# Performance work log

Measured on AMD Instinct MI355X. Metric: run time of the kernel, lower is better.

## Reference

```python
import jax, jax.numpy as jnp
import numpy as np

HIDDEN = 4096
FFN = 14336
GS = 64  # groupsize


def dequant2(qw, scales, zeros, N):
    """Unpack 2-bit HQQ weights. qw: (N//4, K) int32, scales/zeros: (G, K).
    Returns W of shape (N, K) float: (bits - zeros[n % G]) * scales[n % G]."""
    G = scales.shape[0]
    n = jnp.arange(N)
    packed = qw[n // 4]                      # (N, K)
    shift = ((3 - (n % 4)) * 2).astype(qw.dtype)  # per-row bit shift
    vals = (packed >> shift[:, None]) & 3    # (N, K) 2-bit codes
    g = n % G
    return (vals.astype(scales.dtype) - zeros[g]) * scales[g]


def setup_inputs() -> dict:
    key = jax.random.key(0)
    ks = jax.random.split(key, 12)
    x = jax.random.normal(ks[0], (512, HIDDEN), dtype=jnp.float32)
    qw1 = jax.random.randint(ks[1], (FFN // 4, HIDDEN), 0, 256, dtype=jnp.int32)
    qw3 = jax.random.randint(ks[2], (FFN // 4, HIDDEN), 0, 256, dtype=jnp.int32)
    qw2 = jax.random.randint(ks[3], (HIDDEN // 4, FFN), 0, 256, dtype=jnp.int32)
    G1 = FFN // GS
    G2 = HIDDEN // GS
    s1 = jax.random.uniform(ks[4], (G1, HIDDEN), dtype=jnp.float32) * 0.05
    z1 = jax.random.uniform(ks[5], (G1, HIDDEN), dtype=jnp.float32)
    s3 = jax.random.uniform(ks[6], (G1, HIDDEN), dtype=jnp.float32) * 0.05
    z3 = jax.random.uniform(ks[7], (G1, HIDDEN), dtype=jnp.float32)
    s2 = jax.random.uniform(ks[8], (G2, FFN), dtype=jnp.float32) * 0.05
    z2 = jax.random.uniform(ks[9], (G2, FFN), dtype=jnp.float32)
    return {"x": x, "qw1": qw1, "s1": s1, "z1": z1, "qw3": qw3, "s3": s3,
            "z3": z3, "qw2": qw2, "s2": s2, "z2": z2, "groupsize": GS}


def reference(x, qw1, s1, z1, qw3, s3, z3, qw2, s2, z2, groupsize):
    # gate / up projections: C = x @ W^T, W dequantized to (N, K)
    w1 = dequant2(qw1, s1, z1, FFN)      # (FFN, HIDDEN)
    w3 = dequant2(qw3, s3, z3, FFN)      # (FFN, HIDDEN)
    w2 = dequant2(qw2, s2, z2, HIDDEN)   # (HIDDEN, FFN)
    gate = jnp.einsum('mk,nk->mn', x, w1)   # (M, FFN)
    up = jnp.einsum('mk,nk->mn', x, w3)     # (M, FFN)
    h = jax.nn.silu(gate) * up               # SwiGLU
    out = jnp.einsum('mf,hf->mh', h, w2)     # (M, HIDDEN)
    return out
```

## Files before the change

### kernel.cpp

```cpp
#include <hip/hip_runtime.h>
#include <hip/hip_fp16.h>
#include <stdint.h>

#define HIDDEN 4096
#define FFN    14336
#define MDIM   512
#define G1     224
#define G2     64
#define BK     64
#define KB_H   128
#define KB_F   448

typedef _Float16 f16x8 __attribute__((ext_vector_type(8)));
typedef float f32x4 __attribute__((ext_vector_type(4)));

#define SCHED0() __builtin_amdgcn_sched_barrier(0);
#define LGKM_BAR()                                            \
    asm volatile("s_waitcnt lgkmcnt(0)" ::: "memory");        \
    __builtin_amdgcn_s_barrier();                             \
    __builtin_amdgcn_sched_barrier(0);


__global__ void cvt_xp_kernel(const float* __restrict__ x, ushort* __restrict__ xbp) {
    int i = blockIdx.x * blockDim.x + threadIdx.x;
    int ls = i & 63;
    int kb = (i >> 6) & (KB_H - 1);
    int mb = i >> 13;
    int row = mb * 16 + (ls & 15);
    int col = kb * 32 + (ls >> 4) * 8;
    const float4* src = (const float4*)&x[(size_t)row * HIDDEN + col];
    float4 v0 = src[0], v1 = src[1];
    __half2 h0 = __floats2half2_rn(v0.x, v0.y);
    __half2 h1 = __floats2half2_rn(v0.z, v0.w);
    __half2 h2 = __floats2half2_rn(v1.x, v1.y);
    __half2 h3 = __floats2half2_rn(v1.z, v1.w);
    uint4 o = make_uint4(__builtin_bit_cast(uint32_t, h0), __builtin_bit_cast(uint32_t, h1),
                         __builtin_bit_cast(uint32_t, h2), __builtin_bit_cast(uint32_t, h3));
    ((uint4*)xbp)[i] = o;
}

__global__ void build_sz_kernel(const float* __restrict__ s, const float* __restrict__ z,
                                uint32_t* __restrict__ outp) {
    int i = blockIdx.x * blockDim.x + threadIdx.x;
    float s0 = s[2 * i], s1 = s[2 * i + 1];
    float z0 = z[2 * i], z1 = z[2 * i + 1];
    __half2 hs = __floats2half2_rn(s0, s1);
    __half2 hn = __floats2half2_rn(-z0 * s0, -z1 * s1);
    ((uint2*)outp)[i] = make_uint2(__builtin_bit_cast(uint32_t, hs),
                                   __builtin_bit_cast(uint32_t, hn));
}

__device__ __forceinline__ uint32_t deq2(uint32_t w0, uint32_t w1, uint32_t sh,
                                         uint32_t spair, uint32_t npair) {
    uint32_t c0 = (w0 >> sh) & 3u;
    uint32_t c1 = (w1 >> sh) & 3u;
    uint32_t sel = 0x01000100u + c0 * 0x0202u + c1 * 0x02020000u;
    uint32_t codes = __builtin_amdgcn_perm(0x42004000u, 0x3C000000u, sel);
    __half2 r = __hfma2(__builtin_bit_cast(__half2, codes),
                        __builtin_bit_cast(__half2, spair),
                        __builtin_bit_cast(__half2, npair));
    return __builtin_bit_cast(uint32_t, r);
}


__global__ __launch_bounds__(256, 2)
void gemm_gateup(const ushort* __restrict__ xbp, const uint32_t* __restrict__ qw1,
                 const uint32_t* __restrict__ sz1, const uint32_t* __restrict__ qw3,
                 const uint32_t* __restrict__ sz3, ushort* __restrict__ hp) {
    __shared__ ushort sB1[2][32 * 64];
    __shared__ ushort sB2[2][32 * 64];
    __shared__ ushort sE[256 * 32];

    const int tid = threadIdx.x;
    const int idx = ((blockIdx.x & 7) * 112) + (blockIdx.x >> 3);
    const int mt = idx & 1, nt = idx >> 1;
    const int m0 = mt * 256, n0 = nt * 32;

    const int lane = tid & 63, w = tid >> 6;
    const int wm = w * 64;
    const int frow = lane & 15, fk = (lane >> 4) * 8;
    const int sw = (frow & 7) << 3;

    uint32_t abase[4];
#pragma unroll
    for (int mi = 0; mi < 4; ++mi)
        abase[mi] = (uint32_t)(((m0 >> 4) + w * 4 + mi) * KB_H) * 512 + lane * 8;

    const int bi = tid & 127;
    const int rp = bi >> 3;
    const int kc = (bi & 7) * 8;
    const int row0 = rp * 2;
    const int g0 = (n0 + row0) % G1;
    const uint32_t* qp = (tid < 128 ? qw1 : qw3) + (size_t)(n0 / 4 + (rp >> 1)) * HIDDEN + kc;
    const uint32_t* zp = (tid < 128 ? sz1 : sz3) + (size_t)g0 * HIDDEN + kc;
    ushort (*sB)[32 * 64] = (tid < 128) ? sB1 : sB2;
    const uint32_t sh0 = 6u - 4u * (uint32_t)(rp & 1);

    f32x4 accG[4][2], accU[4][2];
#pragma unroll
    for (int i = 0; i < 4; ++i)
#pragma unroll
        for (int j = 0; j < 2; ++j) {
            accG[i][j] = (f32x4){0.f, 0.f, 0.f, 0.f};
            accU[i][j] = (f32x4){0.f, 0.f, 0.f, 0.f};
        }

    f16x8 afA[8], afB[8];
    uint4 pwA0, pwA1, pzA0, pzA1, pzA2, pzA3;
    uint4 pwB0, pwB1, pzB0, pzB1, pzB2, pzB3;

#define GU_LDA(AF, tt)                                                         \
    { _Pragma("unroll")                                                        \
      for (int mi = 0; mi < 4; ++mi)                                           \
          _Pragma("unroll")                                                    \
          for (int kk = 0; kk < 2; ++kk)                                       \
              AF[mi * 2 + kk] =                                                \
                  *(const f16x8*)&xbp[abase[mi] + (uint32_t)((tt) * 2 + kk) * 512]; }

#define GU_LD(PW0, PW1, PZ0, PZ1, PZ2, PZ3, k0q)                               \
    PW0 = *(const uint4*)(qp + (k0q));                                         \
    PW1 = *(const uint4*)(qp + (k0q) + 4);                                     \
    PZ0 = *(const uint4*)(zp + (k0q));                                         \
    PZ1 = *(const uint4*)(zp + (k0q) + 4);                                     \
    PZ2 = *(const uint4*)(zp + HIDDEN + (k0q));                                \
    PZ3 = *(const uint4*)(zp + HIDDEN + (k0q) + 4);

#define GU_DEQ(wbuf, PW0, PW1, PZ0, PZ1, PZ2, PZ3)                             \
    { const uint32_t wv[8] = {(PW0).x, (PW0).y, (PW0).z, (PW0).w,              \
                              (PW1).x, (PW1).y, (PW1).z, (PW1).w};             \
      {   const uint32_t sp[4] = {(PZ0).x, (PZ0).z, (PZ1).x, (PZ1).z};         \
          const uint32_t np[4] = {(PZ0).y, (PZ0).w, (PZ1).y, (PZ1).w};         \
          uint32_t o[4];                                                       \
          _Pragma("unroll")                                                    \
          for (int j = 0; j < 4; ++j)                                          \
              o[j] = deq2(wv[2*j], wv[2*j+1], sh0, sp[j], np[j]);              \
          *(uint4*)&sB[wbuf][row0 * 64 + (kc ^ ((row0 & 7) << 3))] =           \
              make_uint4(o[0], o[1], o[2], o[3]);                              \
      }                                                                        \
      {   const uint32_t sp[4] = {(PZ2).x, (PZ2).z, (PZ3).x, (PZ3).z};         \
          const uint32_t np[4] = {(PZ2).y, (PZ2).w, (PZ3).y, (PZ3).w};         \
          uint32_t o[4];                                                       \
          _Pragma("unroll")                                                    \
          for (int j = 0; j < 4; ++j)                                          \
              o[j] = deq2(wv[2*j], wv[2*j+1], sh0 - 2u, sp[j], np[j]);         \
          const int row1 = row0 + 1;                                           \
          *(uint4*)&sB[wbuf][row1 * 64 + (kc ^ ((row1 & 7) << 3))] =           \
              make_uint4(o[0], o[1], o[2], o[3]);                              \
      } }

#define GU_COMP(AF, rbuf)                                                      \
    { _Pragma("unroll")                                                        \
      for (int kk = 0; kk < 2; ++kk) {                                         \
          const int col = ((kk * 32) + fk) ^ sw;                               \
          f16x8 bg0 = *(const f16x8*)&sB1[rbuf][frow * 64 + col];              \
          f16x8 bg1 = *(const f16x8*)&sB1[rbuf][(16 + frow) * 64 + col];       \
          f16x8 bu0 = *(const f16x8*)&sB2[rbuf][frow * 64 + col];              \
          f16x8 bu1 = *(const f16x8*)&sB2[rbuf][(16 + frow) * 64 + col];       \
          _Pragma("unroll")                                                    \
          for (int mi = 0; mi < 4; ++mi) {                                     \
              accG[mi][0] = __builtin_amdgcn_mfma_f32_16x16x32_f16(AF[mi*2+kk], bg0, accG[mi][0], 0, 0, 0); \
              accG[mi][1] = __builtin_amdgcn_mfma_f32_16x16x32_f16(AF[mi*2+kk], bg1, accG[mi][1], 0, 0, 0); \
              accU[mi][0] = __builtin_amdgcn_mfma_f32_16x16x32_f16(AF[mi*2+kk], bu0, accU[mi][0], 0, 0, 0); \
              accU[mi][1] = __builtin_amdgcn_mfma_f32_16x16x32_f16(AF[mi*2+kk], bu1, accU[mi][1], 0, 0, 0); \
          } } }

#define GU_STEP(tcur, AFW, AFR, WBUF, RBUF, PW0, PW1, PZ0, PZ1, PZ2, PZ3, DOLDA, DOLQ) \
    { if (DOLDA) { GU_LDA(AFW, (tcur) + 1) } SCHED0()                          \
      GU_DEQ(WBUF, PW0, PW1, PZ0, PZ1, PZ2, PZ3)                               \
      if (DOLQ) { GU_LD(PW0, PW1, PZ0, PZ1, PZ2, PZ3, ((tcur) + 3) * BK) }     \
      GU_COMP(AFR, RBUF)                                                       \
      LGKM_BAR() }

    GU_LD(pwA0, pwA1, pzA0, pzA1, pzA2, pzA3, 0)
    GU_LDA(afA, 0)
    GU_DEQ(0, pwA0, pwA1, pzA0, pzA1, pzA2, pzA3)
    GU_LD(pwA0, pwA1, pzA0, pzA1, pzA2, pzA3, BK)
    GU_LD(pwB0, pwB1, pzB0, pzB1, pzB2, pzB3, 2 * BK)
    LGKM_BAR()

    for (int t = 0; t < 60; t += 2) {
        GU_STEP(t,     afB, afA, 1, 0, pwA0, pwA1, pzA0, pzA1, pzA2, pzA3, 1, 1)
        GU_STEP(t + 1, afA, afB, 0, 1, pwB0, pwB1, pzB0, pzB1, pzB2, pzB3, 1, 1)
    }
    GU_STEP(60, afB, afA, 1, 0, pwA0, pwA1, pzA0, pzA1, pzA2, pzA3, 1, 1)
    GU_STEP(61, afA, afB, 0, 1, pwB0, pwB1, pzB0, pzB1, pzB2, pzB3, 1, 0)
    GU_STEP(62, afB, afA, 1, 0, pwA0, pwA1, pzA0, pzA1, pzA2, pzA3, 1, 0)
    GU_COMP(afB, 1)

    const int rb = (lane >> 4) * 4, cb = lane & 15;
#pragma unroll
    for (int mi = 0; mi < 4; ++mi)
#pragma unroll
        for (int ni = 0; ni < 2; ++ni) {
            f32x4 g = accG[mi][ni], u = accU[mi][ni];
            const int row = wm + mi * 16 + rb;
            const int colx = ni * 16 + cb;
#pragma unroll
            for (int r = 0; r < 4; ++r) {
                float gv = g[r];
                float hv = __fdividef(gv, 1.0f + __expf(-gv)) * u[r];
                __half hh = __float2half(hv);
                sE[(row + r) * 32 + colx] = __builtin_bit_cast(ushort, hh);
            }
        }
    __syncthreads();
    {
#pragma unroll
        for (int j = 0; j < 4; ++j) {
            const int slot = tid + j * 256;
            const int mbi = slot >> 6, ls = slot & 63;
            uint4 v = *(const uint4*)&sE[(mbi * 16 + (ls & 15)) * 32 + (ls >> 4) * 8];
            *(uint4*)&hp[(size_t)(((m0 >> 4) + mbi) * KB_F + nt) * 512 + ls * 8] = v;
        }
    }
#undef GU_LDA
#undef GU_LD
#undef GU_DEQ
#undef GU_COMP
#undef GU_STEP
}


__global__ __launch_bounds__(256, 2)
void gemm_down(const ushort* __restrict__ hp, const uint32_t* __restrict__ qw2,
               const uint32_t* __restrict__ sz2, float* __restrict__ part) {
    __shared__ ushort sBd[2][32 * 64];

    const int tid = threadIdx.x;
    const int idx = ((blockIdx.x & 7) * 64) + (blockIdx.x >> 3);
    const int mt = idx & 1, nt = (idx >> 1) & 127, sk = idx >> 8;
    const int m0 = mt * 256, n0 = nt * 32;
    const int kb0 = sk * 224;

    const int lane = tid & 63, w = tid >> 6;
    const int wm = w * 64;
    const int frow = lane & 15, fk = (lane >> 4) * 8;
    const int sw = (frow & 7) << 3;

    uint32_t abase[4];
#pragma unroll
    for (int mi = 0; mi < 4; ++mi)
        abase[mi] = (uint32_t)(((m0 >> 4) + w * 4 + mi) * KB_F + kb0) * 512 + lane * 8;

    const int r = tid >> 3;
    const int kc = (tid & 7) * 8;
    const int g = ((nt & 1) * 32) + r;
    const int kbeg = sk * (FFN / 2);
    const uint32_t* qp = qw2 + (size_t)(n0 / 4 + (r >> 2)) * FFN + kbeg + kc;
    const uint32_t* zp = sz2 + (size_t)g * FFN + kbeg + kc;
    const uint32_t sh = 6u - 2u * (uint32_t)(r & 3);

    f32x4 acc[4][2];
#pragma unroll
    for (int i = 0; i < 4; ++i)
#pragma unroll
        for (int j = 0; j < 2; ++j) acc[i][j] = (f32x4){0.f, 0.f, 0.f, 0.f};

    f16x8 afA[8], afB[8];
    uint4 pwA0, pwA1, pzA0, pzA1;
    uint4 pwB0, pwB1, pzB0, pzB1;

#define GD_LDA(AF, tt)                                                         \
    { _Pragma("unroll")                                                        \
      for (int mi = 0; mi < 4; ++mi)                                           \
          _Pragma("unroll")                                                    \
          for (int kk = 0; kk < 2; ++kk)                                       \
              AF[mi * 2 + kk] =                                                \
                  *(const f16x8*)&hp[abase[mi] + (uint32_t)((tt) * 2 + kk) * 512]; }

#define GD_LD(PW0, PW1, PZ0, PZ1, k0q)                                         \
    PW0 = *(const uint4*)(qp + (k0q));                                         \
    PW1 = *(const uint4*)(qp + (k0q) + 4);                                     \
    PZ0 = *(const uint4*)(zp + (k0q));                                         \
    PZ1 = *(const uint4*)(zp + (k0q) + 4);

#define GD_DEQ(wbuf, PW0, PW1, PZ0, PZ1)                                       \
    { const uint32_t wv[8] = {(PW0).x, (PW0).y, (PW0).z, (PW0).w,              \
                              (PW1).x, (PW1).y, (PW1).z, (PW1).w};             \
      const uint32_t sp[4] = {(PZ0).x, (PZ0).z, (PZ1).x, (PZ1).z};             \
      const uint32_t np[4] = {(PZ0).y, (PZ0).w, (PZ1).y, (PZ1).w};             \
      uint32_t o[4];                                                           \
      _Pragma("unroll")                                                        \
      for (int j = 0; j < 4; ++j)                                              \
          o[j] = deq2(wv[2*j], wv[2*j+1], sh, sp[j], np[j]);                   \
      *(uint4*)&sBd[wbuf][r * 64 + (kc ^ ((r & 7) << 3))] =                    \
          make_uint4(o[0], o[1], o[2], o[3]); }

#define GD_COMP(AF, rbuf)                                                      \
    { _Pragma("unroll")                                                        \
      for (int kk = 0; kk < 2; ++kk) {                                         \
          const int col = ((kk * 32) + fk) ^ sw;                               \
          f16x8 bf0 = *(const f16x8*)&sBd[rbuf][frow * 64 + col];              \
          f16x8 bf1 = *(const f16x8*)&sBd[rbuf][(16 + frow) * 64 + col];       \
          _Pragma("unroll")                                                    \
          for (int mi = 0; mi < 4; ++mi) {                                     \
              acc[mi][0] = __builtin_amdgcn_mfma_f32_16x16x32_f16(AF[mi*2+kk], bf0, acc[mi][0], 0, 0, 0); \
              acc[mi][1] = __builtin_amdgcn_mfma_f32_16x16x32_f16(AF[mi*2+kk], bf1, acc[mi][1], 0, 0, 0); \
          } } }

#define GD_STEP(tcur, AFW, AFR, WBUF, RBUF, PW0, PW1, PZ0, PZ1, DOLDA, DOLQ)   \
    { if (DOLDA) { GD_LDA(AFW, (tcur) + 1) } SCHED0()                          \
      GD_DEQ(WBUF, PW0, PW1, PZ0, PZ1)                                         \
      if (DOLQ) { GD_LD(PW0, PW1, PZ0, PZ1, ((tcur) + 3) * BK) }               \
      GD_COMP(AFR, RBUF)                                                       \
      LGKM_BAR() }

    GD_LD(pwA0, pwA1, pzA0, pzA1, 0)
    GD_LDA(afA, 0)
    GD_DEQ(0, pwA0, pwA1, pzA0, pzA1)
    GD_LD(pwA0, pwA1, pzA0, pzA1, BK)
    GD_LD(pwB0, pwB1, pzB0, pzB1, 2 * BK)
    LGKM_BAR()

    for (int t = 0; t < 108; t += 2) {
        GD_STEP(t,     afB, afA, 1, 0, pwA0, pwA1, pzA0, pzA1, 1, 1)
        GD_STEP(t + 1, afA, afB, 0, 1, pwB0, pwB1, pzB0, pzB1, 1, 1)
    }
    GD_STEP(108, afB, afA, 1, 0, pwA0, pwA1, pzA0, pzA1, 1, 1)
    GD_STEP(109, afA, afB, 0, 1, pwB0, pwB1, pzB0, pzB1, 1, 0)
    GD_STEP(110, afB, afA, 1, 0, pwA0, pwA1, pzA0, pzA1, 1, 0)
    GD_COMP(afB, 1)

    float* pp = part + (size_t)sk * MDIM * HIDDEN;
    const int rb = (lane >> 4) * 4, cb = lane & 15;
#pragma unroll
    for (int mi = 0; mi < 4; ++mi)
#pragma unroll
        for (int ni = 0; ni < 2; ++ni) {
            f32x4 a = acc[mi][ni];
            const int mm = m0 + wm + mi * 16 + rb;
            const int nn = n0 + ni * 16 + cb;
#pragma unroll
            for (int rr = 0; rr < 4; ++rr) pp[(size_t)(mm + rr) * HIDDEN + nn] = a[rr];
        }
#undef GD_LDA
#undef GD_LD
#undef GD_DEQ
#undef GD_COMP
#undef GD_STEP
}


__global__ void reduce_out(const float* __restrict__ part, float* __restrict__ out) {
    int i = blockIdx.x * blockDim.x + threadIdx.x;
    const int Q = MDIM * HIDDEN / 4;
    float4 a = ((const float4*)part)[i];
    float4 b = ((const float4*)part)[i + Q];
    float4 o;
    o.x = a.x + b.x; o.y = a.y + b.y; o.z = a.z + b.z; o.w = a.w + b.w;
    ((float4*)out)[i] = o;
}


extern "C" void kernel_launch(void* const* d_in, const int* in_sizes, int n_in,
                              void* d_out, int out_size, void* d_ws, size_t ws_size,
                              hipStream_t stream) {
    (void)in_sizes; (void)n_in; (void)out_size; (void)ws_size;

    const float* x  = (const float*)d_in[0];
    const uint32_t* qw1 = (const uint32_t*)d_in[1];
    const float* s1 = (const float*)d_in[2];
    const float* z1 = (const float*)d_in[3];
    const uint32_t* qw3 = (const uint32_t*)d_in[4];
    const float* s3 = (const float*)d_in[5];
    const float* z3 = (const float*)d_in[6];
    const uint32_t* qw2 = (const uint32_t*)d_in[7];
    const float* s2 = (const float*)d_in[8];
    const float* z2 = (const float*)d_in[9];
    float* out = (float*)d_out;

    char* ws = (char*)d_ws;
    ushort*   xbp  = (ushort*)ws;
    uint32_t* szp1 = (uint32_t*)(ws + (size_t)MDIM * HIDDEN * 2);
    uint32_t* szp3 = szp1 + (size_t)G1 * HIDDEN;
    uint32_t* szp2 = szp3 + (size_t)G1 * HIDDEN;
    ushort*   hp   = (ushort*)(szp2 + (size_t)G2 * FFN);
    float*    part = (float*)((char*)hp + (size_t)MDIM * FFN * 2);

    cvt_xp_kernel<<<(MDIM * HIDDEN / 8) / 256, 256, 0, stream>>>(x, xbp);
    build_sz_kernel<<<(G1 * HIDDEN / 2) / 256, 256, 0, stream>>>(s1, z1, szp1);
    build_sz_kernel<<<(G1 * HIDDEN / 2) / 256, 256, 0, stream>>>(s3, z3, szp3);
    build_sz_kernel<<<(G2 * FFN / 2) / 256, 256, 0, stream>>>(s2, z2, szp2);

    gemm_gateup<<<(FFN / 32) * (MDIM / 256), 256, 0, stream>>>(xbp, qw1, szp1, qw3, szp3, hp);
    gemm_down<<<2 * (MDIM / 256) * (HIDDEN / 32), 256, 0, stream>>>(hp, qw2, szp2, part);
    reduce_out<<<(MDIM * HIDDEN / 4) / 256, 256, 0, stream>>>(part, out);
}
```

Before: 285.2 us.

## Double K-tile to 128 and restructure pipeline with per-kk A-fragment prefetch

After: 376.1 us. +31.9%, slower.

```diff
diff --git a/kernel.cpp b/kernel.cpp
--- a/kernel.cpp
+++ b/kernel.cpp
@@ -7,7 +7,7 @@
 #define MDIM   512
 #define G1     224
 #define G2     64
-#define BK     64
+#define BK     128
 #define KB_H   128
 #define KB_F   448
 
@@ -62,13 +62,26 @@
     return __builtin_bit_cast(uint32_t, r);
 }
 
+__device__ __forceinline__ void deq_row16(const uint32_t* wv, const uint4* zva, uint32_t sh,
+                                          ushort* dst0, ushort* dst1) {
+    uint32_t o[8];
+#pragma unroll
+    for (int j = 0; j < 8; ++j) {
+        uint32_t sp = (j & 1) ? zva[j >> 1].z : zva[j >> 1].x;
+        uint32_t np = (j & 1) ? zva[j >> 1].w : zva[j >> 1].y;
+        o[j] = deq2(wv[2 * j], wv[2 * j + 1], sh, sp, np);
+    }
+    *(uint4*)dst0 = make_uint4(o[0], o[1], o[2], o[3]);
+    *(uint4*)dst1 = make_uint4(o[4], o[5], o[6], o[7]);
+}
+
 
 __global__ __launch_bounds__(256, 2)
 void gemm_gateup(const ushort* __restrict__ xbp, const uint32_t* __restrict__ qw1,
                  const uint32_t* __restrict__ sz1, const uint32_t* __restrict__ qw3,
                  const uint32_t* __restrict__ sz3, ushort* __restrict__ hp) {
-    __shared__ ushort sB1[2][32 * 64];
-    __shared__ ushort sB2[2][32 * 64];
+    __shared__ ushort sB1[2][32 * 128];
+    __shared__ ushort sB2[2][32 * 128];
     __shared__ ushort sE[256 * 32];
 
     const int tid = threadIdx.x;
@@ -88,13 +101,17 @@
 
     const int bi = tid & 127;
     const int rp = bi >> 3;
-    const int kc = (bi & 7) * 8;
+    const int kc = (bi & 7) * 16;
     const int row0 = rp * 2;
     const int g0 = (n0 + row0) % G1;
     const uint32_t* qp = (tid < 128 ? qw1 : qw3) + (size_t)(n0 / 4 + (rp >> 1)) * HIDDEN + kc;
     const uint32_t* zp = (tid < 128 ? sz1 : sz3) + (size_t)g0 * HIDDEN + kc;
-    ushort (*sB)[32 * 64] = (tid < 128) ? sB1 : sB2;
+    ushort (*sB)[32 * 128] = (tid < 128) ? sB1 : sB2;
     const uint32_t sh0 = 6u - 4u * (uint32_t)(rp & 1);
+    const int wc0 = row0 * 128 + (kc ^ ((row0 & 7) << 3));
+    const int wc1 = row0 * 128 + ((kc + 8) ^ ((row0 & 7) << 3));
+    const int wc2 = (row0 + 1) * 128 + (kc ^ (((row0 + 1) & 7) << 3));
+    const int wc3 = (row0 + 1) * 128 + ((kc + 8) ^ (((row0 + 1) & 7) << 3));
 
     f32x4 accG[4][2], accU[4][2];
 #pragma unroll
@@ -105,87 +122,72 @@
             accU[i][j] = (f32x4){0.f, 0.f, 0.f, 0.f};
         }
 
-    f16x8 afA[8], afB[8];
-    uint4 pwA0, pwA1, pzA0, pzA1, pzA2, pzA3;
-    uint4 pwB0, pwB1, pzB0, pzB1, pzB2, pzB3;
-
-#define GU_LDA(AF, tt)                                                         \
+    f16x8 afE[4], afO[4];
+    uint4 qv0, qv1, qv2, qv3;
+    uint4 zv0, zv1, zv2, zv3;
+    uint4 zv4, zv5, zv6, zv7;
+
+#define GU_LDA(AF, kbidx)                                                      \
     { _Pragma("unroll")                                                        \
       for (int mi = 0; mi < 4; ++mi)                                           \
-          _Pragma("unroll")                                                    \
-          for (int kk = 0; kk < 2; ++kk)                                       \
-              AF[mi * 2 + kk] =                                                \
-                  *(const f16x8*)&xbp[abase[mi] + (uint32_t)((tt) * 2 + kk) * 512]; }
-
-#define GU_LD(PW0, PW1, PZ0, PZ1, PZ2, PZ3, k0q)                               \
-    PW0 = *(const uint4*)(qp + (k0q));                                         \
-    PW1 = *(const uint4*)(qp + (k0q) + 4);                                     \
-    PZ0 = *(const uint4*)(zp + (k0q));                                         \
-    PZ1 = *(const uint4*)(zp + (k0q) + 4);                                     \
-    PZ2 = *(const uint4*)(zp + HIDDEN + (k0q));                                \
-    PZ3 = *(const uint4*)(zp + HIDDEN + (k0q) + 4);
-
-#define GU_DEQ(wbuf, PW0, PW1, PZ0, PZ1, PZ2, PZ3)                             \
-    { const uint32_t wv[8] = {(PW0).x, (PW0).y, (PW0).z, (PW0).w,              \
-                              (PW1).x, (PW1).y, (PW1).z, (PW1).w};             \
-      {   const uint32_t sp[4] = {(PZ0).x, (PZ0).z, (PZ1).x, (PZ1).z};         \
-          const uint32_t np[4] = {(PZ0).y, (PZ0).w, (PZ1).y, (PZ1).w};         \
-          uint32_t o[4];                                                       \
-          _Pragma("unroll")                                                    \
-          for (int j = 0; j < 4; ++j)                                          \
-              o[j] = deq2(wv[2*j], wv[2*j+1], sh0, sp[j], np[j]);              \
-          *(uint4*)&sB[wbuf][row0 * 64 + (kc ^ ((row0 & 7) << 3))] =           \
-              make_uint4(o[0], o[1], o[2], o[3]);                              \
-      }                                                                        \
-      {   const uint32_t sp[4] = {(PZ2).x, (PZ2).z, (PZ3).x, (PZ3).z};         \
-          const uint32_t np[4] = {(PZ2).y, (PZ2).w, (PZ3).y, (PZ3).w};         \
-          uint32_t o[4];                                                       \
-          _Pragma("unroll")                                                    \
-          for (int j = 0; j < 4; ++j)                                          \
-              o[j] = deq2(wv[2*j], wv[2*j+1], sh0 - 2u, sp[j], np[j]);         \
-          const int row1 = row0 + 1;                                           \
-          *(uint4*)&sB[wbuf][row1 * 64 + (kc ^ ((row1 & 7) << 3))] =           \
-              make_uint4(o[0], o[1], o[2], o[3]);                              \
+          AF[mi] = *(const f16x8*)&xbp[abase[mi] + (uint32_t)(kbidx) * 512]; }
+
+#define GU_LDQZ(k0q)                                                           \
+    qv0 = *(const uint4*)(qp + (k0q));      qv1 = *(const uint4*)(qp + (k0q) + 4);  \
+    qv2 = *(const uint4*)(qp + (k0q) + 8);  qv3 = *(const uint4*)(qp + (k0q) + 12); \
+    zv0 = *(const uint4*)(zp + (k0q));      zv1 = *(const uint4*)(zp + (k0q) + 4);  \
+    zv2 = *(const uint4*)(zp + (k0q) + 8);  zv3 = *(const uint4*)(zp + (k0q) + 12); \
+    zv4 = *(const uint4*)(zp + HIDDEN + (k0q));      zv5 = *(const uint4*)(zp + HIDDEN + (k0q) + 4); \
+    zv6 = *(const uint4*)(zp + HIDDEN + (k0q) + 8);  zv7 = *(const uint4*)(zp + HIDDEN + (k0q) + 12);
+
+#define GU_DEQ(wbuf)                                                           \
+    { const uint32_t wv[16] = {qv0.x, qv0.y, qv0.z, qv0.w, qv1.x, qv1.y, qv1.z, qv1.w, \
+                               qv2.x, qv2.y, qv2.z, qv2.w, qv3.x, qv3.y, qv3.z, qv3.w}; \
+      { const uint4 zva[4] = {zv0, zv1, zv2, zv3};                             \
+        deq_row16(wv, zva, sh0, &sB[wbuf][wc0], &sB[wbuf][wc1]); }             \
+      { const uint4 zva[4] = {zv4, zv5, zv6, zv7};                             \
+        deq_row16(wv, zva, sh0 - 2u, &sB[wbuf][wc2], &sB[wbuf][wc3]); } }
+
+#define GU_MFMA_KK(AF, rbuf, kk)                                               \
+    { const int col = ((kk) * 32 + fk) ^ sw;                                   \
+      f16x8 bg0 = *(const f16x8*)&sB1[rbuf][frow * 128 + col];                 \
+      f16x8 bg1 = *(const f16x8*)&sB1[rbuf][(16 + frow) * 128 + col];          \
+      f16x8 bu0 = *(const f16x8*)&sB2[rbuf][frow * 128 + col];                 \
+      f16x8 bu1 = *(const f16x8*)&sB2[rbuf][(16 + frow) * 128 + col];          \
+      _Pragma("unroll")                                                        \
+      for (int mi = 0; mi < 4; ++mi) {                                         \
+          accG[mi][0] = __builtin_amdgcn_mfma_f32_16x16x32_f16(AF[mi], bg0, accG[mi][0], 0, 0, 0); \
+          accG[mi][1] = __builtin_amdgcn_mfma_f32_16x16x32_f16(AF[mi], bg1, accG[mi][1], 0, 0, 0); \
+          accU[mi][0] = __builtin_amdgcn_mfma_f32_16x16x32_f16(AF[mi], bu0, accU[mi][0], 0, 0, 0); \
+          accU[mi][1] = __builtin_amdgcn_mfma_f32_16x16x32_f16(AF[mi], bu1, accU[mi][1], 0, 0, 0); \
       } }
 
-#define GU_COMP(AF, rbuf)                                                      \
-    { _Pragma("unroll")                                                        \
-      for (int kk = 0; kk < 2; ++kk) {                                         \
-          const int col = ((kk * 32) + fk) ^ sw;                               \
-          f16x8 bg0 = *(const f16x8*)&sB1[rbuf][frow * 64 + col];              \
-          f16x8 bg1 = *(const f16x8*)&sB1[rbuf][(16 + frow) * 64 + col];       \
-          f16x8 bu0 = *(const f16x8*)&sB2[rbuf][frow * 64 + col];              \
-          f16x8 bu1 = *(const f16x8*)&sB2[rbuf][(16 + frow) * 64 + col];       \
-          _Pragma("unroll")                                                    \
-          for (int mi = 0; mi < 4; ++mi) {                                     \
-              accG[mi][0] = __builtin_amdgcn_mfma_f32_16x16x32_f16(AF[mi*2+kk], bg0, accG[mi][0], 0, 0, 0); \
-              accG[mi][1] = __builtin_amdgcn_mfma_f32_16x16x32_f16(AF[mi*2+kk], bg1, accG[mi][1], 0, 0, 0); \
-              accU[mi][0] = __builtin_amdgcn_mfma_f32_16x16x32_f16(AF[mi*2+kk], bu0, accU[mi][0], 0, 0, 0); \
-              accU[mi][1] = __builtin_amdgcn_mfma_f32_16x16x32_f16(AF[mi*2+kk], bu1, accU[mi][1], 0, 0, 0); \
-          } } }
-
-#define GU_STEP(tcur, AFW, AFR, WBUF, RBUF, PW0, PW1, PZ0, PZ1, PZ2, PZ3, DOLDA, DOLQ) \
-    { if (DOLDA) { GU_LDA(AFW, (tcur) + 1) } SCHED0()                          \
-      GU_DEQ(WBUF, PW0, PW1, PZ0, PZ1, PZ2, PZ3)                               \
-      if (DOLQ) { GU_LD(PW0, PW1, PZ0, PZ1, PZ2, PZ3, ((tcur) + 3) * BK) }     \
-      GU_COMP(AFR, RBUF)                                                       \
-      LGKM_BAR() }
-
-    GU_LD(pwA0, pwA1, pzA0, pzA1, pzA2, pzA3, 0)
-    GU_LDA(afA, 0)
-    GU_DEQ(0, pwA0, pwA1, pzA0, pzA1, pzA2, pzA3)
-    GU_LD(pwA0, pwA1, pzA0, pzA1, pzA2, pzA3, BK)
-    GU_LD(pwB0, pwB1, pzB0, pzB1, pzB2, pzB3, 2 * BK)
+#define GU_COMP(tcur, rbuf, DON)                                               \
+    { GU_LDA(afO, (tcur) * 4 + 1)                                              \
+      GU_MFMA_KK(afE, rbuf, 0)                                                 \
+      GU_LDA(afE, (tcur) * 4 + 2)                                              \
+      GU_MFMA_KK(afO, rbuf, 1)                                                 \
+      GU_LDA(afO, (tcur) * 4 + 3)                                              \
+      GU_MFMA_KK(afE, rbuf, 2)                                                 \
+      if (DON) { GU_LDA(afE, (tcur) * 4 + 4) }                                 \
+      GU_MFMA_KK(afO, rbuf, 3) }
+
+    GU_LDA(afE, 0)
+    GU_LDQZ(0)
+    GU_DEQ(0)
+    SCHED0()
+    GU_LDQZ(BK)
     LGKM_BAR()
 
-    for (int t = 0; t < 60; t += 2) {
-        GU_STEP(t,     afB, afA, 1, 0, pwA0, pwA1, pzA0, pzA1, pzA2, pzA3, 1, 1)
-        GU_STEP(t + 1, afA, afB, 0, 1, pwB0, pwB1, pzB0, pzB1, pzB2, pzB3, 1, 1)
+    for (int t = 0; t < 31; ++t) {
+        GU_DEQ((t + 1) & 1)
+        SCHED0()
+        if (t <= 29) { GU_LDQZ((t + 2) * BK) }
+        SCHED0()
+        GU_COMP(t, t & 1, 1)
+        LGKM_BAR()
     }
-    GU_STEP(60, afB, afA, 1, 0, pwA0, pwA1, pzA0, pzA1, pzA2, pzA3, 1, 1)
-    GU_STEP(61, afA, afB, 0, 1, pwB0, pwB1, pzB0, pzB1, pzB2, pzB3, 1, 0)
-    GU_STEP(62, afB, afA, 1, 0, pwA0, pwA1, pzA0, pzA1, pzA2, pzA3, 1, 0)
-    GU_COMP(afB, 1)
+    GU_COMP(31, 1, 0)
 
     const int rb = (lane >> 4) * 4, cb = lane & 15;
 #pragma unroll
@@ -214,23 +216,24 @@
         }
     }
 #undef GU_LDA
-#undef GU_LD
+#undef GU_LDQZ
 #undef GU_DEQ
+#undef GU_MFMA_KK
 #undef GU_COMP
-#undef GU_STEP
-}
-
-
-__global__ __launch_bounds__(256, 2)
+}
+
+
+__global__ __launch_bounds__(256, 3)
 void gemm_down(const ushort* __restrict__ hp, const uint32_t* __restrict__ qw2,
                const uint32_t* __restrict__ sz2, float* __restrict__ part) {
-    __shared__ ushort sBd[2][32 * 64];
+    __shared__ ushort sBd[2][32 * 128];
 
     const int tid = threadIdx.x;
     const int idx = ((blockIdx.x & 7) * 64) + (blockIdx.x >> 3);
     const int mt = idx & 1, nt = (idx >> 1) & 127, sk = idx >> 8;
     const int m0 = mt * 256, n0 = nt * 32;
     const int kb0 = sk * 224;
+    const int kbeg = sk * (FFN / 2);
 
     const int lane = tid & 63, w = tid >> 6;
     const int wm = w * 64;
@@ -243,12 +246,13 @@
         abase[mi] = (uint32_t)(((m0 >> 4) + w * 4 + mi) * KB_F + kb0) * 512 + lane * 8;
 
     const int r = tid >> 3;
-    const int kc = (tid & 7) * 8;
+    const int kc = (tid & 7) * 16;
     const int g = ((nt & 1) * 32) + r;
-    const int kbeg = sk * (FFN / 2);
     const uint32_t* qp = qw2 + (size_t)(n0 / 4 + (r >> 2)) * FFN + kbeg + kc;
     const uint32_t* zp = sz2 + (size_t)g * FFN + kbeg + kc;
     const uint32_t sh = 6u - 2u * (uint32_t)(r & 3);
+    const int wc0 = r * 128 + (kc ^ ((r & 7) << 3));
+    const int wc1 = r * 128 + ((kc + 8) ^ ((r & 7) << 3));
 
     f32x4 acc[4][2];
 #pragma unroll
@@ -256,70 +260,63 @@
 #pragma unroll
         for (int j = 0; j < 2; ++j) acc[i][j] = (f32x4){0.f, 0.f, 0.f, 0.f};
 
-    f16x8 afA[8], afB[8];
-    uint4 pwA0, pwA1, pzA0, pzA1;
-    uint4 pwB0, pwB1, pzB0, pzB1;
-
-#define GD_LDA(AF, tt)                                                         \
+    f16x8 afE[4], afO[4];
+    uint4 qv0, qv1, qv2, qv3;
+    uint4 zv0, zv1, zv2, zv3;
+
+#define GD_LDA(AF, kbidx)                                                      \
     { _Pragma("unroll")                                                        \
       for (int mi = 0; mi < 4; ++mi)                                           \
-          _Pragma("unroll")                                                    \
-          for (int kk = 0; kk < 2; ++kk)                                       \
-              AF[mi * 2 + kk] =                                                \
-                  *(const f16x8*)&hp[abase[mi] + (uint32_t)((tt) * 2 + kk) * 512]; }
-
-#define GD_LD(PW0, PW1, PZ0, PZ1, k0q)                                         \
-    PW0 = *(const uint4*)(qp + (k0q));                                         \
-    PW1 = *(const uint4*)(qp + (k0q) + 4);                                     \
-    PZ0 = *(const uint4*)(zp + (k0q));                                         \
-    PZ1 = *(const uint4*)(zp + (k0q) + 4);
-
-#define GD_DEQ(wbuf, PW0, PW1, PZ0, PZ1)                                       \
-    { const uint32_t wv[8] = {(PW0).x, (PW0).y, (PW0).z, (PW0).w,              \
-                              (PW1).x, (PW1).y, (PW1).z, (PW1).w};             \
-      const uint32_t sp[4] = {(PZ0).x, (PZ0).z, (PZ1).x, (PZ1).z};             \
-      const uint32_t np[4] = {(PZ0).y, (PZ0).w, (PZ1).y, (PZ1).w};             \
-      uint32_t o[4];                                                           \
+          AF[mi] = *(const f16x8*)&hp[abase[mi] + (uint32_t)(kbidx) * 512]; }
+
+#define GD_LDQZ(k0q)                                                           \
+    qv0 = *(const uint4*)(qp + (k0q));      qv1 = *(const uint4*)(qp + (k0q) + 4);  \
+    qv2 = *(const uint4*)(qp + (k0q) + 8);  qv3 = *(const uint4*)(qp + (k0q) + 12); \
+    zv0 = *(const uint4*)(zp + (k0q));      zv1 = *(const uint4*)(zp + (k0q) + 4);  \
+    zv2 = *(const uint4*)(zp + (k0q) + 8);  zv3 = *(const uint4*)(zp + (k0q) + 12);
+
+#define GD_DEQ(wbuf)                                                           \
+    { const uint32_t wv[16] = {qv0.x, qv0.y, qv0.z, qv0.w, qv1.x, qv1.y, qv1.z, qv1.w, \
+                               qv2.x, qv2.y, qv2.z, qv2.w, qv3.x, qv3.y, qv3.z, qv3.w}; \
+      const uint4 zva[4] = {zv0, zv1, zv2, zv3};                               \
+      deq_row16(wv, zva, sh, &sBd[wbuf][wc0], &sBd[wbuf][wc1]); }
+
+#define GD_MFMA_KK(AF, rbuf, kk)                                               \
+    { const int col = ((kk) * 32 + fk) ^ sw;                                   \
+      f16x8 bf0 = *(const f16x8*)&sBd[rbuf][frow * 128 + col];                 \
+      f16x8 bf1 = *(const f16x8*)&sBd[rbuf][(16 + frow) * 128 + col];          \
       _Pragma("unroll")                                                        \
-      for (int j = 0; j < 4; ++j)                                              \
-          o[j] = deq2(wv[2*j], wv[2*j+1], sh, sp[j], np[j]);                   \
-      *(uint4*)&sBd[wbuf][r * 64 + (kc ^ ((r & 7) << 3))] =                    \
-          make_uint4(o[0], o[1], o[2], o[3]); }
-
-#define GD_COMP(AF, rbuf)                                                      \
-    { _Pragma("unroll")                                                        \
-      for (int kk = 0; kk < 2; ++kk) {                                         \
-          const int col = ((kk * 32) + fk) ^ sw;                               \
-          f16x8 bf0 = *(const f16x8*)&sBd[rbuf][frow * 64 + col];              \
-          f16x8 bf1 = *(const f16x8*)&sBd[rbuf][(16 + frow) * 64 + col];       \
-          _Pragma("unroll")                                                    \
-          for (int mi = 0; mi < 4; ++mi) {                                     \
-              acc[mi][0] = __builtin_amdgcn_mfma_f32_16x16x32_f16(AF[mi*2+kk], bf0, acc[mi][0], 0, 0, 0); \
-              acc[mi][1] = __builtin_amdgcn_mfma_f32_16x16x32_f16(AF[mi*2+kk], bf1, acc[mi][1], 0, 0, 0); \
-          } } }
-
-#define GD_STEP(tcur, AFW, AFR, WBUF, RBUF, PW0, PW1, PZ0, PZ1, DOLDA, DOLQ)   \
-    { if (DOLDA) { GD_LDA(AFW, (tcur) + 1) } SCHED0()                          \
-      GD_DEQ(WBUF, PW0, PW1, PZ0, PZ1)                                         \
-      if (DOLQ) { GD_LD(PW0, PW1, PZ0, PZ1, ((tcur) + 3) * BK) }               \
-      GD_COMP(AFR, RBUF)                                                       \
-      LGKM_BAR() }
-
-    GD_LD(pwA0, pwA1, pzA0, pzA1, 0)
-    GD_LDA(afA, 0)
-    GD_DEQ(0, pwA0, pwA1, pzA0, pzA1)
-    GD_LD(pwA0, pwA1, pzA0, pzA1, BK)
-    GD_LD(pwB0, pwB1, pzB0, pzB1, 2 * BK)
+      for (int mi = 0; mi < 4; ++mi) {                                         \
+          acc[mi][0] = __builtin_amdgcn_mfma_f32_16x16x32_f16(AF[mi], bf0, acc[mi][0], 0, 0, 0); \
+          acc[mi][1] = __builtin_amdgcn_mfma_f32_16x16x32_f16(AF[mi], bf1, acc[mi][1], 0, 0, 0); \
+      } }
+
+#define GD_COMP(tcur, rbuf, DON)                                               \
+    { GD_LDA(afO, (tcur) * 4 + 1)                                              \
+      GD_MFMA_KK(afE, rbuf, 0)                                                 \
+      GD_LDA(afE, (tcur) * 4 + 2)                                               \
+      GD_MFMA_KK(afO, rbuf, 1)                                                 \
+      GD_LDA(afO, (tcur) * 4 + 3)                                              \
+      GD_MFMA_KK(afE, rbuf, 2)                                                 \
+      if (DON) { GD_LDA(afE, (tcur) * 4 + 4) }                                 \
+      GD_MFMA_KK(afO, rbuf, 3) }
+
+    GD_LDA(afE, 0)
+    GD_LDQZ(0)
+    GD_DEQ(0)
+    SCHED0()
+    GD_LDQZ(BK)
     LGKM_BAR()
 
-    for (int t = 0; t < 108; t += 2) {
-        GD_STEP(t,     afB, afA, 1, 0, pwA0, pwA1, pzA0, pzA1, 1, 1)
-        GD_STEP(t + 1, afA, afB, 0, 1, pwB0, pwB1, pzB0, pzB1, 1, 1)
+    for (int t = 0; t < 55; ++t) {
+        GD_DEQ((t + 1) & 1)
+        SCHED0()
+        if (t <= 53) { GD_LDQZ((t + 2) * BK) }
+        SCHED0()
+        GD_COMP(t, t & 1, 1)
+        LGKM_BAR()
     }
-    GD_STEP(108, afB, afA, 1, 0, pwA0, pwA1, pzA0, pzA1, 1, 1)
-    GD_STEP(109, afA, afB, 0, 1, pwB0, pwB1, pzB0, pzB1, 1, 0)
-    GD_STEP(110, afB, afA, 1, 0, pwA0, pwA1, pzA0, pzA1, 1, 0)
-    GD_COMP(afB, 1)
+    GD_COMP(55, 1, 0)
 
     float* pp = part + (size_t)sk * MDIM * HIDDEN;
     const int rb = (lane >> 4) * 4, cb = lane & 15;
@@ -334,10 +331,10 @@
             for (int rr = 0; rr < 4; ++rr) pp[(size_t)(mm + rr) * HIDDEN + nn] = a[rr];
         }
 #undef GD_LDA
-#undef GD_LD
+#undef GD_LDQZ
 #undef GD_DEQ
+#undef GD_MFMA_KK
 #undef GD_COMP
-#undef GD_STEP
 }
 
 
```

## Fuse prep kernels and replace split-K partial buffer with atomic adds

Applied to the files above, without the earlier changes.

Measured after the change: 293.1 us. 1.03x slower.

```diff
diff --git a/kernel.cpp b/kernel.cpp
--- a/kernel.cpp
+++ b/kernel.cpp
@@ -20,34 +20,46 @@
     __builtin_amdgcn_s_barrier();                             \
     __builtin_amdgcn_sched_barrier(0);
 
-
-__global__ void cvt_xp_kernel(const float* __restrict__ x, ushort* __restrict__ xbp) {
-    int i = blockIdx.x * blockDim.x + threadIdx.x;
-    int ls = i & 63;
-    int kb = (i >> 6) & (KB_H - 1);
-    int mb = i >> 13;
-    int row = mb * 16 + (ls & 15);
-    int col = kb * 32 + (ls >> 4) * 8;
-    const float4* src = (const float4*)&x[(size_t)row * HIDDEN + col];
-    float4 v0 = src[0], v1 = src[1];
-    __half2 h0 = __floats2half2_rn(v0.x, v0.y);
-    __half2 h1 = __floats2half2_rn(v0.z, v0.w);
-    __half2 h2 = __floats2half2_rn(v1.x, v1.y);
-    __half2 h3 = __floats2half2_rn(v1.z, v1.w);
-    uint4 o = make_uint4(__builtin_bit_cast(uint32_t, h0), __builtin_bit_cast(uint32_t, h1),
-                         __builtin_bit_cast(uint32_t, h2), __builtin_bit_cast(uint32_t, h3));
-    ((uint4*)xbp)[i] = o;
-}
-
-__global__ void build_sz_kernel(const float* __restrict__ s, const float* __restrict__ z,
-                                uint32_t* __restrict__ outp) {
-    int i = blockIdx.x * blockDim.x + threadIdx.x;
-    float s0 = s[2 * i], s1 = s[2 * i + 1];
-    float z0 = z[2 * i], z1 = z[2 * i + 1];
-    __half2 hs = __floats2half2_rn(s0, s1);
-    __half2 hn = __floats2half2_rn(-z0 * s0, -z1 * s1);
-    ((uint2*)outp)[i] = make_uint2(__builtin_bit_cast(uint32_t, hs),
-                                   __builtin_bit_cast(uint32_t, hn));
+__global__ void prep_fused(const float* __restrict__ x,
+                           const float* __restrict__ s1, const float* __restrict__ z1,
+                           const float* __restrict__ s3, const float* __restrict__ z3,
+                           const float* __restrict__ s2, const float* __restrict__ z2,
+                           ushort* __restrict__ xbp, uint32_t* __restrict__ szp1,
+                           uint32_t* __restrict__ szp3, uint32_t* __restrict__ szp2,
+                           float* __restrict__ out) {
+    const int b = blockIdx.x, t = threadIdx.x;
+    if (b < 1024) {
+        int i = b * 256 + t;
+        int ls = i & 63;
+        int kb = (i >> 6) & (KB_H - 1);
+        int mb = i >> 13;
+        int row = mb * 16 + (ls & 15);
+        int col = kb * 32 + (ls >> 4) * 8;
+        const float4* src = (const float4*)&x[(size_t)row * HIDDEN + col];
+        float4 v0 = src[0], v1 = src[1];
+        __half2 h0 = __floats2half2_rn(v0.x, v0.y);
+        __half2 h1 = __floats2half2_rn(v0.z, v0.w);
+        __half2 h2 = __floats2half2_rn(v1.x, v1.y);
+        __half2 h3 = __floats2half2_rn(v1.z, v1.w);
+        ((uint4*)xbp)[i] = make_uint4(
+            __builtin_bit_cast(uint32_t, h0), __builtin_bit_cast(uint32_t, h1),
+            __builtin_bit_cast(uint32_t, h2), __builtin_bit_cast(uint32_t, h3));
+    } else if (b < 6400) {
+        const int seg = (b - 1024) / 1792;
+        const int i = (b - 1024 - seg * 1792) * 256 + t;
+        const float* sp = (seg == 0) ? s1 : (seg == 1) ? s3 : s2;
+        const float* zp = (seg == 0) ? z1 : (seg == 1) ? z3 : z2;
+        uint32_t* op = (seg == 0) ? szp1 : (seg == 1) ? szp3 : szp2;
+        float sv0 = sp[2 * i], sv1 = sp[2 * i + 1];
+        float zv0 = zp[2 * i], zv1 = zp[2 * i + 1];
+        __half2 hs = __floats2half2_rn(sv0, sv1);
+        __half2 hn = __floats2half2_rn(-zv0 * sv0, -zv1 * sv1);
+        ((uint2*)op)[i] = make_uint2(__builtin_bit_cast(uint32_t, hs),
+                                     __builtin_bit_cast(uint32_t, hn));
+    } else {
+        int i = (b - 6400) * 256 + t;
+        ((float4*)out)[i] = make_float4(0.f, 0.f, 0.f, 0.f);
+    }
 }
 
 __device__ __forceinline__ uint32_t deq2(uint32_t w0, uint32_t w1, uint32_t sh,
@@ -223,7 +235,7 @@
 
 __global__ __launch_bounds__(256, 2)
 void gemm_down(const ushort* __restrict__ hp, const uint32_t* __restrict__ qw2,
-               const uint32_t* __restrict__ sz2, float* __restrict__ part) {
+               const uint32_t* __restrict__ sz2, float* __restrict__ out) {
     __shared__ ushort sBd[2][32 * 64];
 
     const int tid = threadIdx.x;
@@ -231,6 +243,7 @@
     const int mt = idx & 1, nt = (idx >> 1) & 127, sk = idx >> 8;
     const int m0 = mt * 256, n0 = nt * 32;
     const int kb0 = sk * 224;
+    const int kbeg = sk * (FFN / 2);
 
     const int lane = tid & 63, w = tid >> 6;
     const int wm = w * 64;
@@ -245,7 +258,6 @@
     const int r = tid >> 3;
     const int kc = (tid & 7) * 8;
     const int g = ((nt & 1) * 32) + r;
-    const int kbeg = sk * (FFN / 2);
     const uint32_t* qp = qw2 + (size_t)(n0 / 4 + (r >> 2)) * FFN + kbeg + kc;
     const uint32_t* zp = sz2 + (size_t)g * FFN + kbeg + kc;
     const uint32_t sh = 6u - 2u * (uint32_t)(r & 3);
@@ -321,7 +333,6 @@
     GD_STEP(110, afB, afA, 1, 0, pwA0, pwA1, pzA0, pzA1, 1, 0)
     GD_COMP(afB, 1)
 
-    float* pp = part + (size_t)sk * MDIM * HIDDEN;
     const int rb = (lane >> 4) * 4, cb = lane & 15;
 #pragma unroll
     for (int mi = 0; mi < 4; ++mi)
@@ -331,24 +342,14 @@
             const int mm = m0 + wm + mi * 16 + rb;
             const int nn = n0 + ni * 16 + cb;
 #pragma unroll
-            for (int rr = 0; rr < 4; ++rr) pp[(size_t)(mm + rr) * HIDDEN + nn] = a[rr];
+            for (int rr = 0; rr < 4; ++rr)
+                atomicAdd(&out[(size_t)(mm + rr) * HIDDEN + nn], a[rr]);
         }
 #undef GD_LDA
 #undef GD_LD
 #undef GD_DEQ
 #undef GD_COMP
 #undef GD_STEP
-}
-
-
-__global__ void reduce_out(const float* __restrict__ part, float* __restrict__ out) {
-    int i = blockIdx.x * blockDim.x + threadIdx.x;
-    const int Q = MDIM * HIDDEN / 4;
-    float4 a = ((const float4*)part)[i];
-    float4 b = ((const float4*)part)[i + Q];
-    float4 o;
-    o.x = a.x + b.x; o.y = a.y + b.y; o.z = a.z + b.z; o.w = a.w + b.w;
-    ((float4*)out)[i] = o;
 }
 
 
@@ -375,14 +376,9 @@
     uint32_t* szp3 = szp1 + (size_t)G1 * HIDDEN;
     uint32_t* szp2 = szp3 + (size_t)G1 * HIDDEN;
     ushort*   hp   = (ushort*)(szp2 + (size_t)G2 * FFN);
-    float*    part = (float*)((char*)hp + (size_t)MDIM * FFN * 2);
-
-    cvt_xp_kernel<<<(MDIM * HIDDEN / 8) / 256, 256, 0, stream>>>(x, xbp);
-    build_sz_kernel<<<(G1 * HIDDEN / 2) / 256, 256, 0, stream>>>(s1, z1, szp1);
-    build_sz_kernel<<<(G1 * HIDDEN / 2) / 256, 256, 0, stream>>>(s3, z3, szp3);
-    build_sz_kernel<<<(G2 * FFN / 2) / 256, 256, 0, stream>>>(s2, z2, szp2);
-
+
+    prep_fused<<<8448, 256, 0, stream>>>(x, s1, z1, s3, z3, s2, z2,
+                                         xbp, szp1, szp3, szp2, out);
     gemm_gateup<<<(FFN / 32) * (MDIM / 256), 256, 0, stream>>>(xbp, qw1, szp1, qw3, szp3, hp);
-    gemm_down<<<2 * (MDIM / 256) * (HIDDEN / 32), 256, 0, stream>>>(hp, qw2, szp2, part);
-    reduce_out<<<(MDIM * HIDDEN / 4) / 256, 256, 0, stream>>>(part, out);
-}
+    gemm_down<<<2 * (MDIM / 256) * (HIDDEN / 32), 256, 0, stream>>>(hp, qw2, szp2, out);
+}
```
